# Kernel optimization log

Hardware: AMD Instinct MI355X
Metric: run time of the kernel (lower is better)

Reference implementation:

```python
import jax, jax.numpy as jnp
import numpy as np

DIM = 4096
NUM_EXPERTS = 64
TOP_K = 8
TOKENS = 16384

def setup_inputs() -> dict:
    key = jax.random.key(0)
    kx, kw = jax.random.split(key)
    x = jax.random.normal(kx, (TOKENS, DIM), dtype=jnp.float32)
    # gate weight as in nn.Linear(dim, num_experts, bias=False): shape [num_experts, dim]
    W = jax.random.normal(kw, (NUM_EXPERTS, DIM), dtype=jnp.float32) * 0.02
    return {"x": x, "W": W}

def reference(x, W):
    # logits = x @ W^T : [tokens, num_experts]
    logits = jnp.einsum('td,ed->te', x, W)
    top_k_values, top_k_indices = jax.lax.top_k(logits, TOP_K)
    # softmax over top-k values in float32, cast back to x dtype
    scores = jax.nn.softmax(top_k_values.astype(jnp.float32), axis=-1).astype(x.dtype)
    return scores, top_k_indices
```

## Files before the change

### kernel.cpp

```cpp
#include <hip/hip_runtime.h>
#include <math.h>

typedef float  f32x4 __attribute__((ext_vector_type(4)));
typedef short  s16x8 __attribute__((ext_vector_type(8)));
typedef unsigned short u16x8 __attribute__((ext_vector_type(8)));
typedef unsigned int   u32x4 __attribute__((ext_vector_type(4)));

constexpr int TOKENS  = 16384;
constexpr int DIM     = 4096;
constexpr int NE      = 64;
constexpr int TOPK    = 8;
constexpr int KB      = 32;
constexpr int NIT     = DIM / KB;
constexpr int LISTCAP = 16384;
constexpr float GAPTH = 1e-4f;

constexpr unsigned WARR_U16   = (unsigned)NIT * 4 * 64 * 8;
constexpr size_t   WS_INT_OFF = (size_t)WARR_U16 * 2 * sizeof(unsigned short);
constexpr size_t   WS_NEEDED  = WS_INT_OFF + sizeof(int) * (size_t)(16 + LISTCAP);

__device__ __forceinline__ unsigned short bf_rne(float f) {
    unsigned u = __float_as_uint(f);
    u += 0x7FFFu + ((u >> 16) & 1u);
    return (unsigned short)(u >> 16);
}
__device__ __forceinline__ float bf_f32(unsigned short h) {
    return __uint_as_float(((unsigned)h) << 16);
}
__device__ __forceinline__ uint2 cvt_pair(float f0, float f1) {
    unsigned short h0 = bf_rne(f0);
    unsigned short h1 = bf_rne(f1);
    uint2 r;
    r.x = (unsigned)h0 | ((unsigned)h1 << 16);
    r.y = (unsigned)bf_rne(f0 - bf_f32(h0)) | ((unsigned)bf_rne(f1 - bf_f32(h1)) << 16);
    return r;
}
union Cvt { u32x4 u; s16x8 s; };

__global__ __launch_bounds__(256)
void wconv_kernel(const float* __restrict__ W, unsigned short* __restrict__ wpk,
                  int* __restrict__ wsI)
{
    unsigned tid = blockIdx.x * 256u + threadIdx.x;
    if (tid == 0) wsI[0] = 0;
    unsigned j    = tid & 7u;
    unsigned lane = (tid >> 3) & 63u;
    unsigned T    = (tid >> 9) & 3u;
    unsigned it   = tid >> 11;
    unsigned e = 16u * T + (lane & 15u);
    unsigned k = 32u * it + 8u * (lane >> 4) + j;
    float v = W[(size_t)e * DIM + k];
    unsigned short h = bf_rne(v);
    wpk[tid]            = h;
    wpk[WARR_U16 + tid] = bf_rne(v - bf_f32(h));
}

__global__ __launch_bounds__(128, 2)
void gemm_topk_v2(const float* __restrict__ x,
                  const unsigned short* __restrict__ wpk,
                  float* __restrict__ out, int* __restrict__ wsI)
{
    __shared__ float ls[32][NE + 4];

    const int t    = threadIdx.x;
    const int w    = t >> 6;
    const int l    = t & 63;
    const int lq   = l >> 4;
    const int ln   = l & 15;
    const int tok0 = blockIdx.x * 32;

    const float* xg = x + (size_t)(tok0 + 16 * w + ln) * DIM + 8 * lq;
    const s16x8* bhp = (const s16x8*)wpk + l;
    const s16x8* blp = bhp + (WARR_U16 / 8);

    f32x4 acc[4];
#pragma unroll
    for (int T = 0; T < 4; ++T) acc[T] = (f32x4){0.f, 0.f, 0.f, 0.f};

    float4 xa0 = *(const float4*)(xg + 0);
    float4 xa1 = *(const float4*)(xg + 4);
    float4 xb0 = *(const float4*)(xg + KB + 0);
    float4 xb1 = *(const float4*)(xg + KB + 4);
    s16x8 bh0 = bhp[0], bh1 = bhp[64], bh2 = bhp[128], bh3 = bhp[192];
    s16x8 bl0 = blp[0], bl1 = blp[64], bl2 = blp[128], bl3 = blp[192];

#pragma unroll 2
    for (int it = 0; it < NIT; ++it) {
        const int itx = (it + 2 < NIT) ? it + 2 : NIT - 1;
        const float* xp = xg + (size_t)KB * itx;
        float4 xn0 = *(const float4*)(xp + 0);
        float4 xn1 = *(const float4*)(xp + 4);

        const int itn = (it + 1 < NIT) ? it + 1 : NIT - 1;
        const s16x8* nhp = bhp + itn * 256;
        const s16x8* nlp = blp + itn * 256;
        s16x8 nh0 = nhp[0], nh1 = nhp[64], nh2 = nhp[128], nh3 = nhp[192];
        s16x8 nl0 = nlp[0], nl1 = nlp[64], nl2 = nlp[128], nl3 = nlp[192];

        uint2 p0 = cvt_pair(xa0.x, xa0.y);
        uint2 p1 = cvt_pair(xa0.z, xa0.w);
        uint2 p2 = cvt_pair(xa1.x, xa1.y);
        uint2 p3 = cvt_pair(xa1.z, xa1.w);
        Cvt ch, cl;
        ch.u = (u32x4){p0.x, p1.x, p2.x, p3.x};
        cl.u = (u32x4){p0.y, p1.y, p2.y, p3.y};
        s16x8 ah = ch.s, al = cl.s;

        acc[0] = __builtin_amdgcn_mfma_f32_16x16x32_bf16(ah, bh0, acc[0], 0, 0, 0);
        acc[1] = __builtin_amdgcn_mfma_f32_16x16x32_bf16(ah, bh1, acc[1], 0, 0, 0);
        acc[2] = __builtin_amdgcn_mfma_f32_16x16x32_bf16(ah, bh2, acc[2], 0, 0, 0);
        acc[3] = __builtin_amdgcn_mfma_f32_16x16x32_bf16(ah, bh3, acc[3], 0, 0, 0);
        acc[0] = __builtin_amdgcn_mfma_f32_16x16x32_bf16(ah, bl0, acc[0], 0, 0, 0);
        acc[1] = __builtin_amdgcn_mfma_f32_16x16x32_bf16(ah, bl1, acc[1], 0, 0, 0);
        acc[2] = __builtin_amdgcn_mfma_f32_16x16x32_bf16(ah, bl2, acc[2], 0, 0, 0);
        acc[3] = __builtin_amdgcn_mfma_f32_16x16x32_bf16(ah, bl3, acc[3], 0, 0, 0);
        acc[0] = __builtin_amdgcn_mfma_f32_16x16x32_bf16(al, bh0, acc[0], 0, 0, 0);
        acc[1] = __builtin_amdgcn_mfma_f32_16x16x32_bf16(al, bh1, acc[1], 0, 0, 0);
        acc[2] = __builtin_amdgcn_mfma_f32_16x16x32_bf16(al, bh2, acc[2], 0, 0, 0);
        acc[3] = __builtin_amdgcn_mfma_f32_16x16x32_bf16(al, bh3, acc[3], 0, 0, 0);

        bh0 = nh0; bh1 = nh1; bh2 = nh2; bh3 = nh3;
        bl0 = nl0; bl1 = nl1; bl2 = nl2; bl3 = nl3;
        xa0 = xb0; xa1 = xb1; xb0 = xn0; xb1 = xn1;
    }

#pragma unroll
    for (int T = 0; T < 4; ++T)
#pragma unroll
        for (int r = 0; r < 4; ++r)
            ls[16 * w + 4 * lq + r][16 * T + ln] = acc[T][r];
    __syncthreads();

    if ((t & 3) == 0) {
        const int ti  = t >> 2;
        const int tok = tok0 + ti;
        float v[9]; int idx[9];
#pragma unroll
        for (int j = 0; j < 9; ++j) {
            float best = -3.4e38f; int bi = 0;
            for (int e = 0; e < NE; ++e) {
                float q = ls[ti][e];
                if (q > best) { best = q; bi = e; }
            }
            v[j] = best; idx[j] = bi;
            ls[ti][bi] = -3.4e38f;
        }
        bool flag = false;
#pragma unroll
        for (int j = 0; j < 8; ++j)
            if (v[j] - v[j + 1] < GAPTH) flag = true;

        float m = v[0], s = 0.f, ex[8];
#pragma unroll
        for (int j = 0; j < 8; ++j) { ex[j] = expf(v[j] - m); s += ex[j]; }
        float inv = 1.f / s;
#pragma unroll
        for (int j = 0; j < 8; ++j) {
            out[(size_t)tok * TOPK + j] = ex[j] * inv;
            out[(size_t)TOKENS * TOPK + (size_t)tok * TOPK + j] = (float)idx[j];
        }
        if (flag) {
            int pos = atomicAdd(wsI, 1);
            if (pos < LISTCAP) wsI[16 + pos] = tok;
        }
    }
}

__global__ __launch_bounds__(256)
void refine_kernel(const float* __restrict__ x, const float* __restrict__ W,
                   float* __restrict__ out, const int* __restrict__ wsI)
{
    __shared__ float  xr[DIM];
    __shared__ double pt[256];
    __shared__ double lg[NE];

    int cnt = wsI[0];
    if (cnt > LISTCAP) cnt = LISTCAP;
    const int t = threadIdx.x;

    for (int g = blockIdx.x; g < cnt; g += gridDim.x) {
        const int tok = wsI[16 + g];
        __syncthreads();
        for (int i = t; i < DIM / 4; i += 256)
            *(float4*)&xr[4 * i] = *(const float4*)&x[(size_t)tok * DIM + 4 * i];
        __syncthreads();

        const int e  = t & 63;
        const int ks = t >> 6;
        const float* wp = W + (size_t)e * DIM + ks * 1024;
        const float* xp = xr + ks * 1024;
        double p = 0.0;
        for (int i = 0; i < 256; ++i) {
            float4 wv = *(const float4*)&wp[4 * i];
            float4 xv = *(const float4*)&xp[4 * i];
            p = fma((double)xv.x, (double)wv.x, p);
            p = fma((double)xv.y, (double)wv.y, p);
            p = fma((double)xv.z, (double)wv.z, p);
            p = fma((double)xv.w, (double)wv.w, p);
        }
        pt[t] = p;
        __syncthreads();
        if (t < NE)
            lg[t] = ((pt[t] + pt[t + 64]) + pt[t + 128]) + pt[t + 192];
        __syncthreads();
        if (t == 0) {
            double vv[8]; int ii[8];
#pragma unroll
            for (int j = 0; j < 8; ++j) {
                double best = -1e300; int bi = 0;
                for (int e2 = 0; e2 < NE; ++e2) {
                    double q = lg[e2];
                    if (q > best) { best = q; bi = e2; }
                }
                vv[j] = best; ii[j] = bi;
                lg[bi] = -1e300;
            }
            float pf[8], ex[8], s = 0.f;
#pragma unroll
            for (int j = 0; j < 8; ++j) pf[j] = (float)vv[j];
            float m = pf[0];
#pragma unroll
            for (int j = 0; j < 8; ++j) { ex[j] = expf(pf[j] - m); s += ex[j]; }
            float inv = 1.f / s;
#pragma unroll
            for (int j = 0; j < 8; ++j) {
                out[(size_t)tok * TOPK + j] = ex[j] * inv;
                out[(size_t)TOKENS * TOPK + (size_t)tok * TOPK + j] = (float)ii[j];
            }
        }
    }
}

__global__ void zero_cnt_kernel(int* wsI) { if (threadIdx.x == 0) wsI[0] = 0; }

__global__ __launch_bounds__(256)
void gemm_topk_old(const float* __restrict__ x, const float* __restrict__ W,
                   float* __restrict__ out, int* __restrict__ wsI)
{
    __shared__ __align__(16) unsigned short frag[8192];
    __shared__ float ls[64][NE + 4];

    const int t    = threadIdx.x;
    const int tok0 = blockIdx.x * 64;

    const int srow = t >> 2;
    const int sq   = t & 3;
    const int sn   = srow & 15;
    const int sT   = srow >> 4;
    const int sdst = sT * 512 + (16 * sq + (sn ^ (2 * sq))) * 8;
    const float* xg = x + (size_t)(tok0 + srow) * DIM + 8 * sq;
    const float* wg = W + (size_t)srow * DIM + 8 * sq;

    const int w  = t >> 6;
    const int l  = t & 63;
    const int lq = l >> 4;
    const int ln = l & 15;
    const int fo = (16 * lq + (ln ^ (2 * lq))) * 8;

    f32x4 acc[4];
#pragma unroll
    for (int T = 0; T < 4; ++T) acc[T] = (f32x4){0.f, 0.f, 0.f, 0.f};

    float4 xa = *(const float4*)xg;
    float4 xb = *(const float4*)(xg + 4);
    float4 wa = *(const float4*)wg;
    float4 wb = *(const float4*)(wg + 4);

    for (int it = 0; it < NIT; ++it) {
        __syncthreads();
        {
            float vx[8] = {xa.x, xa.y, xa.z, xa.w, xb.x, xb.y, xb.z, xb.w};
            float vw[8] = {wa.x, wa.y, wa.z, wa.w, wb.x, wb.y, wb.z, wb.w};
            u16x8 vxh, vxl, vwh, vwl;
#pragma unroll
            for (int j = 0; j < 8; ++j) {
                unsigned short h1 = bf_rne(vx[j]);
                vxh[j] = h1;
                vxl[j] = bf_rne(vx[j] - bf_f32(h1));
                unsigned short h2 = bf_rne(vw[j]);
                vwh[j] = h2;
                vwl[j] = bf_rne(vw[j] - bf_f32(h2));
            }
            *(u16x8*)&frag[   0 + sdst] = vxh;
            *(u16x8*)&frag[2048 + sdst] = vxl;
            *(u16x8*)&frag[4096 + sdst] = vwh;
            *(u16x8*)&frag[6144 + sdst] = vwl;
        }
        __syncthreads();
        if (it + 1 < NIT) {
            const float* xp = xg + (size_t)(it + 1) * KB;
            const float* wp = wg + (size_t)(it + 1) * KB;
            xa = *(const float4*)xp;  xb = *(const float4*)(xp + 4);
            wa = *(const float4*)wp;  wb = *(const float4*)(wp + 4);
        }
        s16x8 ah = *(const s16x8*)&frag[   0 + w * 512 + fo];
        s16x8 al = *(const s16x8*)&frag[2048 + w * 512 + fo];
#pragma unroll
        for (int T = 0; T < 4; ++T) {
            s16x8 bh = *(const s16x8*)&frag[4096 + T * 512 + fo];
            s16x8 bl = *(const s16x8*)&frag[6144 + T * 512 + fo];
            acc[T] = __builtin_amdgcn_mfma_f32_16x16x32_bf16(ah, bh, acc[T], 0, 0, 0);
            acc[T] = __builtin_amdgcn_mfma_f32_16x16x32_bf16(ah, bl, acc[T], 0, 0, 0);
            acc[T] = __builtin_amdgcn_mfma_f32_16x16x32_bf16(al, bh, acc[T], 0, 0, 0);
        }
    }

    __syncthreads();
#pragma unroll
    for (int T = 0; T < 4; ++T)
#pragma unroll
        for (int r = 0; r < 4; ++r)
            ls[16 * w + 4 * lq + r][16 * T + ln] = acc[T][r];
    __syncthreads();

    if (t < 64) {
        const int tok = tok0 + t;
        float v[9]; int idx[9];
#pragma unroll
        for (int j = 0; j < 9; ++j) {
            float best = -3.4e38f; int bi = 0;
            for (int e = 0; e < NE; ++e) {
                float q = ls[t][e];
                if (q > best) { best = q; bi = e; }
            }
            v[j] = best; idx[j] = bi;
            ls[t][bi] = -3.4e38f;
        }
        bool flag = false;
#pragma unroll
        for (int j = 0; j < 8; ++j)
            if (v[j] - v[j + 1] < GAPTH) flag = true;

        float m = v[0], s = 0.f, ex[8];
#pragma unroll
        for (int j = 0; j < 8; ++j) { ex[j] = expf(v[j] - m); s += ex[j]; }
        float inv = 1.f / s;
#pragma unroll
        for (int j = 0; j < 8; ++j) {
            out[(size_t)tok * TOPK + j] = ex[j] * inv;
            out[(size_t)TOKENS * TOPK + (size_t)tok * TOPK + j] = (float)idx[j];
        }
        if (flag) {
            int pos = atomicAdd(wsI, 1);
            if (pos < LISTCAP) wsI[16 + pos] = tok;
        }
    }
}

extern "C" void kernel_launch(void* const* d_in, const int* in_sizes, int n_in,
                              void* d_out, int out_size, void* d_ws, size_t ws_size,
                              hipStream_t stream)
{
    const float* x = (const float*)d_in[0];
    const float* W = (const float*)d_in[1];
    float* out = (float*)d_out;

    if (ws_size >= WS_NEEDED) {
        unsigned short* wpk = (unsigned short*)d_ws;
        int* wsI = (int*)((char*)d_ws + WS_INT_OFF);
        hipLaunchKernelGGL(wconv_kernel, dim3(WARR_U16 / 256), dim3(256), 0, stream, W, wpk, wsI);
        hipLaunchKernelGGL(gemm_topk_v2, dim3(TOKENS / 32), dim3(128), 0, stream, x, wpk, out, wsI);
        hipLaunchKernelGGL(refine_kernel, dim3(256), dim3(256), 0, stream, x, W, out, wsI);
    } else {
        int* wsI = (int*)d_ws;
        hipLaunchKernelGGL(zero_cnt_kernel, dim3(1), dim3(64), 0, stream, wsI);
        hipLaunchKernelGGL(gemm_topk_old, dim3(TOKENS / 64), dim3(256), 0, stream, x, W, out, wsI);
        hipLaunchKernelGGL(refine_kernel, dim3(256), dim3(256), 0, stream, x, W, out, wsI);
    }
}
```

Before: 503.9 us.

## Split K across eight waves per block with LDS partial-sum reduction

The gating GEMM now assigns 16 tokens per 512-thread block, and each of the 8 waves handles a 512-wide slice of the K dimension. The waves' partial logits are summed through shared memory before top-k. This exposes far more waves (1024 blocks of 8 waves instead of 512 blocks of 2) to hide the latency of streaming x, which is memory-bound. The cost is extra LDS traffic and an extra barrier, and top-k now runs on only 16 threads per block.

Measured after the change: 489.9 us. 2.8% less time.

```diff
diff --git a/kernel.cpp b/kernel.cpp
--- a/kernel.cpp
+++ b/kernel.cpp
@@ -12,6 +12,9 @@
 constexpr int TOPK    = 8;
 constexpr int KB      = 32;
 constexpr int NIT     = DIM / KB;
+constexpr int WAVES   = 8;
+constexpr int KSL     = DIM / WAVES;
+constexpr int NITW    = KSL / KB;
 constexpr int LISTCAP = 16384;
 constexpr float GAPTH = 1e-4f;
 
@@ -55,22 +58,23 @@
     wpk[WARR_U16 + tid] = bf_rne(v - bf_f32(h));
 }
 
-__global__ __launch_bounds__(128, 2)
-void gemm_topk_v2(const float* __restrict__ x,
+__global__ __launch_bounds__(512, 8)
+void gemm_topk_v3(const float* __restrict__ x,
                   const unsigned short* __restrict__ wpk,
                   float* __restrict__ out, int* __restrict__ wsI)
 {
-    __shared__ float ls[32][NE + 4];
+    __shared__ float part[WAVES][16][NE + 4];
+    __shared__ float outls[16][NE + 4];
 
     const int t    = threadIdx.x;
-    const int w    = t >> 6;
+    const int ws   = t >> 6;
     const int l    = t & 63;
     const int lq   = l >> 4;
     const int ln   = l & 15;
-    const int tok0 = blockIdx.x * 32;
-
-    const float* xg = x + (size_t)(tok0 + 16 * w + ln) * DIM + 8 * lq;
-    const s16x8* bhp = (const s16x8*)wpk + l;
+    const int tok0 = blockIdx.x * 16;
+
+    const float* xg = x + (size_t)(tok0 + ln) * DIM + ws * KSL + 8 * lq;
+    const s16x8* bhp = (const s16x8*)wpk + ws * NITW * 256 + l;
     const s16x8* blp = bhp + (WARR_U16 / 8);
 
     f32x4 acc[4];
@@ -85,13 +89,13 @@
     s16x8 bl0 = blp[0], bl1 = blp[64], bl2 = blp[128], bl3 = blp[192];
 
 #pragma unroll 2
-    for (int it = 0; it < NIT; ++it) {
-        const int itx = (it + 2 < NIT) ? it + 2 : NIT - 1;
+    for (int it = 0; it < NITW; ++it) {
+        const int itx = (it + 2 < NITW) ? it + 2 : NITW - 1;
         const float* xp = xg + (size_t)KB * itx;
         float4 xn0 = *(const float4*)(xp + 0);
         float4 xn1 = *(const float4*)(xp + 4);
 
-        const int itn = (it + 1 < NIT) ? it + 1 : NIT - 1;
+        const int itn = (it + 1 < NITW) ? it + 1 : NITW - 1;
         const s16x8* nhp = bhp + itn * 256;
         const s16x8* nlp = blp + itn * 256;
         s16x8 nh0 = nhp[0], nh1 = nhp[64], nh2 = nhp[128], nh3 = nhp[192];
@@ -128,22 +132,30 @@
     for (int T = 0; T < 4; ++T)
 #pragma unroll
         for (int r = 0; r < 4; ++r)
-            ls[16 * w + 4 * lq + r][16 * T + ln] = acc[T][r];
+            part[ws][4 * lq + r][16 * T + ln] = acc[T][r];
     __syncthreads();
 
-    if ((t & 3) == 0) {
-        const int ti  = t >> 2;
-        const int tok = tok0 + ti;
+    for (int o = t; o < 16 * NE; o += 512) {
+        const int ti = o >> 6, e = o & 63;
+        float s = 0.f;
+#pragma unroll
+        for (int w2 = 0; w2 < WAVES; ++w2) s += part[w2][ti][e];
+        outls[ti][e] = s;
+    }
+    __syncthreads();
+
+    if (t < 16) {
+        const int tok = tok0 + t;
         float v[9]; int idx[9];
 #pragma unroll
         for (int j = 0; j < 9; ++j) {
             float best = -3.4e38f; int bi = 0;
             for (int e = 0; e < NE; ++e) {
-                float q = ls[ti][e];
+                float q = outls[t][e];
                 if (q > best) { best = q; bi = e; }
             }
             v[j] = best; idx[j] = bi;
-            ls[ti][bi] = -3.4e38f;
+            outls[t][bi] = -3.4e38f;
         }
         bool flag = false;
 #pragma unroll
@@ -359,7 +371,7 @@
         unsigned short* wpk = (unsigned short*)d_ws;
         int* wsI = (int*)((char*)d_ws + WS_INT_OFF);
         hipLaunchKernelGGL(wconv_kernel, dim3(WARR_U16 / 256), dim3(256), 0, stream, W, wpk, wsI);
-        hipLaunchKernelGGL(gemm_topk_v2, dim3(TOKENS / 32), dim3(128), 0, stream, x, wpk, out, wsI);
+        hipLaunchKernelGGL(gemm_topk_v3, dim3(TOKENS / 16), dim3(512), 0, stream, x, wpk, out, wsI);
         hipLaunchKernelGGL(refine_kernel, dim3(256), dim3(256), 0, stream, x, W, out, wsI);
     } else {
         int* wsI = (int*)d_ws;
```
